# Performance work log

Measured on AMD Instinct MI355X. Metric: run time of the kernel, lower is better.

The kernel has to match this reference:

```python
import jax, jax.numpy as jnp
import numpy as np

B, S, D, H = 64, 512, 1024, 1024


def setup_inputs() -> dict:
    key = jax.random.key(0)
    k1, k2, k3 = jax.random.split(key, 3)
    x = jax.random.normal(k1, (B, S, D), dtype=jnp.float32)
    # torch nn.Linear weight: [4H, D+H], bias: [4H]; scale ~ U-like small init
    W = jax.random.normal(k2, (4 * H, D + H), dtype=jnp.float32) * (1.0 / np.sqrt(D + H))
    b = jax.random.normal(k3, (4 * H,), dtype=jnp.float32) * 0.01
    return {"x": x, "W": W, "b": b}


def reference(x, W, b):
    """BaselineLSTM forward (use_ln=False, dropout=Identity).

    Returns (outputs [B,S,H], (h [B,H], c [B,H])).
    """
    Bv, Sv, Dv = x.shape
    Hv = W.shape[0] // 4
    h0 = jnp.zeros((Bv, Hv), dtype=x.dtype)
    c0 = jnp.zeros((Bv, Hv), dtype=x.dtype)

    def step(carry, x_t):
        h, c = carry
        # gates = Linear(cat([x_t, h])) -> [B, 4H], chunk order i,f,o,g
        gates = jnp.concatenate([x_t, h], axis=1) @ W.T + b
        i, f, o, g = jnp.split(gates, 4, axis=1)
        c_new = jax.nn.sigmoid(f) * c + jax.nn.sigmoid(i) * jnp.tanh(g)
        h_new = jax.nn.sigmoid(o) * jnp.tanh(c_new)
        return (h_new, c_new), h_new

    (h, c), outs = jax.lax.scan(step, (h0, c0), jnp.swapaxes(x, 0, 1))
    outputs = jnp.swapaxes(outs, 0, 1)  # [B, S, H]
    return outputs, (h, c)
```

## Files before the change

kernel.cpp:

```cpp
#include <hip/hip_runtime.h>

typedef unsigned short ushort_t;
typedef float  f32x4  __attribute__((ext_vector_type(4)));
typedef __bf16 bf16x8 __attribute__((ext_vector_type(8)));

#define NB   64
#define NS   512
#define ND   1024
#define NH   1024
#define NG   4096
#define WPAD 1032

__device__ __forceinline__ ushort_t f2bf(float f) {
  unsigned u = __float_as_uint(f);
  u += 0x7FFFu + ((u >> 16) & 1u);
  return (ushort_t)(u >> 16);
}
__device__ __forceinline__ float bf2f(ushort_t u) {
  return __uint_as_float(((unsigned)u) << 16);
}
__device__ __forceinline__ float sigmoid_f(float x) {
  return 1.0f / (1.0f + __expf(-x));
}
__device__ __forceinline__ float tanh_f(float x) {
  return 1.0f - 2.0f / (__expf(2.0f * x) + 1.0f);
}

__global__ __launch_bounds__(256) void cvt_x_kernel(const float4* __restrict__ x,
                                                    ushort_t* __restrict__ xb) {
  int i = blockIdx.x * 256 + threadIdx.x;
  float4 v = x[i];
  ushort4 o;
  o.x = f2bf(v.x); o.y = f2bf(v.y); o.z = f2bf(v.z); o.w = f2bf(v.w);
  *(ushort4*)(xb + (size_t)i * 4) = o;
}

__global__ __launch_bounds__(256) void cvt_w_kernel(const float4* __restrict__ W,
                                                    ushort_t* __restrict__ Wx,
                                                    ushort_t* __restrict__ Wh) {
  int i = blockIdx.x * 256 + threadIdx.x;
  float4 v = W[i];
  int e = i * 4;
  int n = e >> 11;
  int c = e & 2047;
  ushort4 o;
  o.x = f2bf(v.x); o.y = f2bf(v.y); o.z = f2bf(v.z); o.w = f2bf(v.w);
  ushort_t* dst = (c < ND) ? (Wx + (size_t)n * ND + c)
                           : (Wh + (size_t)n * NH + (c - ND));
  *(ushort4*)dst = o;
}

__global__ __launch_bounds__(256) void pregemm_kernel(
    const ushort_t* __restrict__ xb, const ushort_t* __restrict__ Wx,
    const float* __restrict__ bias, ushort_t* __restrict__ PG) {
  int bid  = blockIdx.x;
  int mblk = bid >> 5;
  int nblk = bid & 31;
  int tid  = threadIdx.x;
  int lane = tid & 63, w = tid >> 6;
  int l15  = lane & 15, q = lane >> 4;
  int row0 = mblk * 128 + (w >> 1) * 64;
  int col0 = nblk * 128 + (w & 1) * 64;
  const ushort_t* aBase = xb + (size_t)(row0 + l15) * ND + q * 8;
  const ushort_t* bBase = Wx + (size_t)(col0 + l15) * ND + q * 8;

  f32x4 acc[4][4] = {};
#pragma unroll 2
  for (int k0 = 0; k0 < ND; k0 += 32) {
    bf16x8 a[4], b[4];
#pragma unroll
    for (int mi = 0; mi < 4; ++mi)
      a[mi] = *reinterpret_cast<const bf16x8*>(aBase + (size_t)mi * 16 * ND + k0);
#pragma unroll
    for (int ni = 0; ni < 4; ++ni)
      b[ni] = *reinterpret_cast<const bf16x8*>(bBase + (size_t)ni * 16 * ND + k0);
#pragma unroll
    for (int mi = 0; mi < 4; ++mi)
#pragma unroll
      for (int ni = 0; ni < 4; ++ni)
        acc[mi][ni] = __builtin_amdgcn_mfma_f32_16x16x32_bf16(a[mi], b[ni], acc[mi][ni], 0, 0, 0);
  }
#pragma unroll
  for (int ni = 0; ni < 4; ++ni) {
    int n = col0 + ni * 16 + l15;
    float bv = bias[n];
#pragma unroll
    for (int mi = 0; mi < 4; ++mi) {
#pragma unroll
      for (int r = 0; r < 4; ++r) {
        int m  = row0 + mi * 16 + q * 4 + r;
        int bb = m >> 9;
        int t  = m & 511;
        PG[((size_t)t * NB + bb) * NG + n] = f2bf(acc[mi][ni][r] + bv);
      }
    }
  }
}

__global__ __launch_bounds__(1024) void lstm_rec_kernel(
    const ushort_t* __restrict__ PG, const ushort_t* __restrict__ Wh,
    ushort_t* hbuf, unsigned* cnt, float* __restrict__ out) {
  __shared__ ushort_t lds_wh[64 * WPAD];
  __shared__ float lds_g[4][64][17];

  int bid = blockIdx.x;
  int j0  = bid * 16;
  int tid = threadIdx.x;
  int lane = tid & 63, w = tid >> 6;
  int g = w & 3, ms = w >> 2;
  int l15 = lane & 15, q = lane >> 4;
  int jj = tid & 15, m = tid >> 4;

#pragma unroll
  for (int it = 0; it < 8; ++it) {
    int e   = it * 8192 + tid * 8;
    int row = e >> 10;
    int col = e & 1023;
    uint4 v = *(const uint4*)(Wh + ((size_t)((row >> 4) * NH + j0 + (row & 15))) * NH + col);
    *(uint4*)(lds_wh + row * WPAD + col) = v;
  }
  __syncthreads();

  const ushort_t* bBase = lds_wh + (g * 16 + l15) * WPAD + q * 8;
  float c_reg = 0.f;

  ushort_t pg0, pg1, pg2, pg3;
  {
    const ushort_t* pp = PG + (size_t)m * NG + j0 + jj;
    pg0 = pp[0]; pg1 = pp[NH]; pg2 = pp[2 * NH]; pg3 = pp[3 * NH];
  }

  for (int t = 0; t < NS; ++t) {
    if (t > 0) {
      if (tid == 0) {
        unsigned tgt = 64u * (unsigned)t;
        int guard = 0;
        while (__hip_atomic_load(cnt, __ATOMIC_RELAXED, __HIP_MEMORY_SCOPE_AGENT) < tgt) {
          if (++guard > (1 << 16)) break;
        }
        __builtin_amdgcn_fence(__ATOMIC_ACQUIRE, "agent");
      }
      __syncthreads();
    }

    const ushort_t* hb    = hbuf + (size_t)(t & 1) * (NB * NH);
    const ushort_t* aBase = hb + (size_t)(ms * 16 + l15) * NH + q * 8;
    f32x4 acc = {};
#pragma unroll 8
    for (int k0 = 0; k0 < NH; k0 += 32) {
      bf16x8 av = *reinterpret_cast<const bf16x8*>(aBase + k0);
      bf16x8 bv = *reinterpret_cast<const bf16x8*>(bBase + k0);
      acc = __builtin_amdgcn_mfma_f32_16x16x32_bf16(av, bv, acc, 0, 0, 0);
    }
#pragma unroll
    for (int r = 0; r < 4; ++r)
      lds_g[g][ms * 16 + q * 4 + r][l15] = acc[r];
    __syncthreads();

    float gi = lds_g[0][m][jj] + bf2f(pg0);
    float gf = lds_g[1][m][jj] + bf2f(pg1);
    float go = lds_g[2][m][jj] + bf2f(pg2);
    float gg = lds_g[3][m][jj] + bf2f(pg3);
    float cn = sigmoid_f(gf) * c_reg + sigmoid_f(gi) * tanh_f(gg);
    float hv = sigmoid_f(go) * tanh_f(cn);
    c_reg = cn;

    ushort_t* hn = hbuf + (size_t)((t & 1) ^ 1) * (NB * NH);
    hn[(size_t)m * NH + j0 + jj] = f2bf(hv);

    if (t == NS - 1) {
      out[((size_t)m * NS + t) * NH + j0 + jj] = hv;
      out[(size_t)NB * NS * NH + (size_t)m * NH + j0 + jj] = hv;
      out[(size_t)NB * NS * NH + (size_t)NB * NH + (size_t)m * NH + j0 + jj] = cn;
    } else {
      __syncthreads();
      if (tid == 0) {
        __hip_atomic_fetch_add(cnt, 1u, __ATOMIC_RELEASE, __HIP_MEMORY_SCOPE_AGENT);
      }
      __builtin_nontemporal_store(hv, &out[((size_t)m * NS + t) * NH + j0 + jj]);
      const ushort_t* pn = PG + ((size_t)(t + 1) * NB + m) * NG + j0 + jj;
      pg0 = pn[0]; pg1 = pn[NH]; pg2 = pn[2 * NH]; pg3 = pn[3 * NH];
    }
  }
}

extern "C" void kernel_launch(void* const* d_in, const int* in_sizes, int n_in,
                              void* d_out, int out_size, void* d_ws, size_t ws_size,
                              hipStream_t stream) {
  const float* x    = (const float*)d_in[0];
  const float* W    = (const float*)d_in[1];
  const float* bias = (const float*)d_in[2];
  float* out = (float*)d_out;

  const size_t off_hbuf = 0;
  const size_t off_cnt  = 262144;
  const size_t off_Wx   = 262272;
  const size_t off_Wh   = off_Wx + 8388608;
  const size_t off_xb   = off_Wh + 8388608;
  const size_t off_PG   = off_xb + 67108864;
  const size_t need     = off_PG + 268435456;
  if (ws_size < need) return;

  char* ws = (char*)d_ws;
  ushort_t* hbuf = (ushort_t*)(ws + off_hbuf);
  unsigned* cnt  = (unsigned*)(ws + off_cnt);
  ushort_t* Wx   = (ushort_t*)(ws + off_Wx);
  ushort_t* Wh   = (ushort_t*)(ws + off_Wh);
  ushort_t* xb   = (ushort_t*)(ws + off_xb);
  ushort_t* PG   = (ushort_t*)(ws + off_PG);

  hipMemsetAsync(ws, 0, 262272, stream);

  cvt_x_kernel<<<32768, 256, 0, stream>>>((const float4*)x, xb);
  cvt_w_kernel<<<8192, 256, 0, stream>>>((const float4*)W, Wx, Wh);
  pregemm_kernel<<<8192, 256, 0, stream>>>(xb, Wx, bias, PG);

  void* args[] = { (void*)&PG, (void*)&Wh, (void*)&hbuf, (void*)&cnt, (void*)&out };
  hipLaunchCooperativeKernel((void*)lstm_rec_kernel, dim3(64), dim3(1024),
                             args, 0, stream);
}
```

Before: 10.86 ms.

## Stage h in swizzled LDS, stream Wh from global, relax atomics

The recurrent kernel stops keeping its Wh slice in LDS and reads it from global/L2 every step. Instead, each step copies the full bf16 hidden state into XOR-swizzled LDS with relaxed agent-scope atomic loads, and publishes h as packed 32-bit atomic stores. The acquire fence and release ordering on the step counter are dropped to relaxed, the spin guard is shortened, and PG loads become nontemporal. This aims to cut global h-load latency and fence cost on the critical per-step path. The trade is repeated Wh traffic from L2 and weaker memory ordering, which could let blocks read stale h.

```diff
diff --git a/kernel.cpp b/kernel.cpp
--- a/kernel.cpp
+++ b/kernel.cpp
@@ -1,6 +1,7 @@
 #include <hip/hip_runtime.h>
 
 typedef unsigned short ushort_t;
+typedef unsigned long long u64_t;
 typedef float  f32x4  __attribute__((ext_vector_type(4)));
 typedef __bf16 bf16x8 __attribute__((ext_vector_type(8)));
 
@@ -9,7 +10,6 @@
 #define ND   1024
 #define NH   1024
 #define NG   4096
-#define WPAD 1032
 
 __device__ __forceinline__ ushort_t f2bf(float f) {
   unsigned u = __float_as_uint(f);
@@ -100,7 +100,7 @@
 __global__ __launch_bounds__(1024) void lstm_rec_kernel(
     const ushort_t* __restrict__ PG, const ushort_t* __restrict__ Wh,
     ushort_t* hbuf, unsigned* cnt, float* __restrict__ out) {
-  __shared__ ushort_t lds_wh[64 * WPAD];
+  __shared__ ushort_t lds_h[64 * 1024];
   __shared__ float lds_g[4][64][17];
 
   int bid = blockIdx.x;
@@ -111,23 +111,21 @@
   int l15 = lane & 15, q = lane >> 4;
   int jj = tid & 15, m = tid >> 4;
 
-#pragma unroll
-  for (int it = 0; it < 8; ++it) {
-    int e   = it * 8192 + tid * 8;
-    int row = e >> 10;
-    int col = e & 1023;
-    uint4 v = *(const uint4*)(Wh + ((size_t)((row >> 4) * NH + j0 + (row & 15))) * NH + col);
-    *(uint4*)(lds_wh + row * WPAD + col) = v;
-  }
-  __syncthreads();
-
-  const ushort_t* bBase = lds_wh + (g * 16 + l15) * WPAD + q * 8;
+  const ushort_t* bB = Wh + (size_t)(g * NH + j0 + l15) * NH + q * 8;
+
+  int rowA = ms * 16 + l15;
+  int swA  = (rowA & 7) << 4;
+  const char* aRow = (const char*)lds_h + rowA * 2048;
+
   float c_reg = 0.f;
 
   ushort_t pg0, pg1, pg2, pg3;
   {
     const ushort_t* pp = PG + (size_t)m * NG + j0 + jj;
-    pg0 = pp[0]; pg1 = pp[NH]; pg2 = pp[2 * NH]; pg3 = pp[3 * NH];
+    pg0 = __builtin_nontemporal_load(pp);
+    pg1 = __builtin_nontemporal_load(pp + NH);
+    pg2 = __builtin_nontemporal_load(pp + 2 * NH);
+    pg3 = __builtin_nontemporal_load(pp + 3 * NH);
   }
 
   for (int t = 0; t < NS; ++t) {
@@ -136,20 +134,35 @@
         unsigned tgt = 64u * (unsigned)t;
         int guard = 0;
         while (__hip_atomic_load(cnt, __ATOMIC_RELAXED, __HIP_MEMORY_SCOPE_AGENT) < tgt) {
-          if (++guard > (1 << 16)) break;
+          if (++guard > (1 << 14)) break;
         }
-        __builtin_amdgcn_fence(__ATOMIC_ACQUIRE, "agent");
-      }
+      }
+      __builtin_amdgcn_sched_barrier(0);
       __syncthreads();
     }
 
-    const ushort_t* hb    = hbuf + (size_t)(t & 1) * (NB * NH);
-    const ushort_t* aBase = hb + (size_t)(ms * 16 + l15) * NH + q * 8;
+    {
+      const u64_t* hb64 = (const u64_t*)(hbuf + (size_t)(t & 1) * (NB * NH));
+      u64_t hv8[16];
+#pragma unroll
+      for (int it = 0; it < 16; ++it)
+        hv8[it] = __hip_atomic_load(hb64 + it * 1024 + tid,
+                                    __ATOMIC_RELAXED, __HIP_MEMORY_SCOPE_AGENT);
+#pragma unroll
+      for (int it = 0; it < 16; ++it) {
+        int idx  = it * 1024 + tid;
+        int row  = idx >> 8;
+        int colB = (idx & 255) * 8;
+        *(u64_t*)((char*)lds_h + row * 2048 + (colB ^ ((row & 7) << 4))) = hv8[it];
+      }
+    }
+    __syncthreads();
+
     f32x4 acc = {};
 #pragma unroll 8
     for (int k0 = 0; k0 < NH; k0 += 32) {
-      bf16x8 av = *reinterpret_cast<const bf16x8*>(aBase + k0);
-      bf16x8 bv = *reinterpret_cast<const bf16x8*>(bBase + k0);
+      bf16x8 av = *(const bf16x8*)(aRow + ((16 * q + 2 * k0) ^ swA));
+      bf16x8 bv = *reinterpret_cast<const bf16x8*>(bB + k0);
       acc = __builtin_amdgcn_mfma_f32_16x16x32_bf16(av, bv, acc, 0, 0, 0);
     }
 #pragma unroll
@@ -165,21 +178,28 @@
     float hv = sigmoid_f(go) * tanh_f(cn);
     c_reg = cn;
 
-    ushort_t* hn = hbuf + (size_t)((t & 1) ^ 1) * (NB * NH);
-    hn[(size_t)m * NH + j0 + jj] = f2bf(hv);
-
+    unsigned my16 = (unsigned)f2bf(hv);
+    unsigned nb16 = (unsigned)__shfl_down((int)my16, 1);
     if (t == NS - 1) {
       out[((size_t)m * NS + t) * NH + j0 + jj] = hv;
       out[(size_t)NB * NS * NH + (size_t)m * NH + j0 + jj] = hv;
       out[(size_t)NB * NS * NH + (size_t)NB * NH + (size_t)m * NH + j0 + jj] = cn;
     } else {
+      if ((tid & 1) == 0) {
+        unsigned* hn32 = (unsigned*)(hbuf + (size_t)((t & 1) ^ 1) * (NB * NH));
+        __hip_atomic_store(hn32 + m * (NH / 2) + ((j0 + jj) >> 1),
+                           my16 | (nb16 << 16),
+                           __ATOMIC_RELAXED, __HIP_MEMORY_SCOPE_AGENT);
+      }
       __syncthreads();
-      if (tid == 0) {
-        __hip_atomic_fetch_add(cnt, 1u, __ATOMIC_RELEASE, __HIP_MEMORY_SCOPE_AGENT);
-      }
+      if (tid == 0)
+        __hip_atomic_fetch_add(cnt, 1u, __ATOMIC_RELAXED, __HIP_MEMORY_SCOPE_AGENT);
       __builtin_nontemporal_store(hv, &out[((size_t)m * NS + t) * NH + j0 + jj]);
       const ushort_t* pn = PG + ((size_t)(t + 1) * NB + m) * NG + j0 + jj;
-      pg0 = pn[0]; pg1 = pn[NH]; pg2 = pn[2 * NH]; pg3 = pn[3 * NH];
+      pg0 = __builtin_nontemporal_load(pn);
+      pg1 = __builtin_nontemporal_load(pn + NH);
+      pg2 = __builtin_nontemporal_load(pn + 2 * NH);
+      pg3 = __builtin_nontemporal_load(pn + 3 * NH);
     }
   }
 }
```

Result: faster. 10.53 ms (-3.0%).
